# Performance work log

Measured on AMD Instinct MI355X. Metric: run time of the kernel, lower is better.

The kernel has to match this reference:

```python
import jax, jax.numpy as jnp
import numpy as np
import math

N_NODES = 20000
N_EDGES = 320000
NODE_IN = 128
HIDDEN = 64
HEADS = 4
TIME_DIM = 64
SCALE = 60.0 / 1.0  # sensitivity / epsilon


def _linear_params(key, din, dout):
    k1, k2 = jax.random.split(key)
    bound = 1.0 / math.sqrt(din)
    w = jax.random.uniform(k1, (din, dout), minval=-bound, maxval=bound, dtype=jnp.float32)
    b = jax.random.uniform(k2, (dout,), minval=-bound, maxval=bound, dtype=jnp.float32)
    return w, b


def setup_inputs() -> dict:
    key = jax.random.key(0)
    ks = jax.random.split(key, 16)
    edge_index = jax.random.randint(ks[0], (2, N_EDGES), 0, N_NODES, dtype=jnp.int64)
    raw_time = jax.random.uniform(ks[1], (N_EDGES, 1), dtype=jnp.float32) * 86400.0
    noise = jax.random.laplace(ks[2], (N_EDGES, 1), dtype=jnp.float32) * SCALE
    node_emb = jax.random.normal(ks[3], (N_NODES, NODE_IN), dtype=jnp.float32)
    HC = HEADS * HIDDEN
    wq1, bq1 = _linear_params(ks[4], NODE_IN, HC)
    wk1, bk1 = _linear_params(ks[5], NODE_IN, HC)
    wv1, bv1 = _linear_params(ks[6], NODE_IN, HC)
    wt1, bt1 = _linear_params(ks[7], TIME_DIM, HC)
    wq2, bq2 = _linear_params(ks[8], HC, HC)
    wk2, bk2 = _linear_params(ks[9], HC, HC)
    wv2, bv2 = _linear_params(ks[10], HC, HC)
    wt2, bt2 = _linear_params(ks[11], TIME_DIM, HC)
    wc, bc = _linear_params(ks[12], HC, 1)
    return dict(edge_index=edge_index, raw_time=raw_time, noise=noise, node_emb=node_emb,
                wq1=wq1, bq1=bq1, wk1=wk1, bk1=bk1, wv1=wv1, bv1=bv1, wt1=wt1, bt1=bt1,
                wq2=wq2, bq2=bq2, wk2=wk2, bk2=bk2, wv2=wv2, bv2=bv2, wt2=wt2, bt2=bt2,
                wc=wc, bc=bc)


def time_encode(t):
    # t: [E, 1] -> [E, TIME_DIM]; interleaved sin/cos as in TimeEncoder
    half = jnp.arange(0, TIME_DIM, 2, dtype=jnp.float32)
    div_term = jnp.exp(half * (-math.log(10000.0) / TIME_DIM))  # [TIME_DIM/2]
    arg = t * div_term  # [E, TIME_DIM/2]
    te = jnp.stack([jnp.sin(arg), jnp.cos(arg)], axis=-1)  # [E, T/2, 2]
    return te.reshape(t.shape[0], TIME_DIM)


def temporal_conv(x, src, dst, time_enc, wq, bq, wk, bk, wv, bv, wt, bt):
    # gather-QKV, edge softmax over dst segments, scatter-add aggregation
    N = x.shape[0]
    q = (x @ wq + bq).reshape(N, HEADS, HIDDEN)
    k = (x @ wk + bk).reshape(N, HEADS, HIDDEN)
    v = (x @ wv + bv).reshape(N, HEADS, HIDDEN)
    t_enc = (time_enc @ wt + bt).reshape(-1, HEADS, HIDDEN)  # [E,H,C]
    q_i = q[dst]                      # [E,H,C]
    k_j = k[src] + t_enc              # [E,H,C]
    alpha = (q_i * k_j).sum(-1) / math.sqrt(HIDDEN)  # [E,H]
    # segment softmax over index = dst (PyG softmax semantics)
    amax = jax.ops.segment_max(alpha, dst, num_segments=N)  # [N,H]
    ea = jnp.exp(alpha - amax[dst])
    denom = jax.ops.segment_sum(ea, dst, num_segments=N)
    alpha = ea / (denom[dst] + 1e-16)
    msg = v[src] * alpha[..., None]   # [E,H,C]
    out = jax.ops.segment_sum(msg, dst, num_segments=N)  # [N,H,C]
    return out.reshape(N, HEADS * HIDDEN)


def reference(edge_index, raw_time, noise, node_emb,
              wq1, bq1, wk1, bk1, wv1, bv1, wt1, bt1,
              wq2, bq2, wk2, bk2, wv2, bv2, wt2, bt2,
              wc, bc):
    src, dst = edge_index[0], edge_index[1]
    noisy_time = raw_time + noise                 # Laplace mechanism
    time_encoded = time_encode(noisy_time)        # [E, TIME_DIM]
    x = jax.nn.relu(temporal_conv(node_emb, src, dst, time_encoded,
                                  wq1, bq1, wk1, bk1, wv1, bv1, wt1, bt1))
    x = jax.nn.relu(temporal_conv(x, src, dst, time_encoded,
                                  wq2, bq2, wk2, bk2, wv2, bv2, wt2, bt2))
    edge_emb = x[src] + x[dst]                    # [E, H*C]
    out = edge_emb @ wc + bc                      # [E, 1]
    return out.squeeze(-1)
```

## Files before the change

### kernel.cpp

```cpp
#include <hip/hip_runtime.h>
#include <hip/hip_fp16.h>
#include <math.h>

#define NN   20000
#define NE   320000
#define NIN  128
#define HC   256
#define NB   1024

typedef unsigned short u16;
typedef __attribute__((ext_vector_type(8))) short bf16x8;
typedef __attribute__((ext_vector_type(8))) unsigned short u16x8;
typedef __attribute__((ext_vector_type(4))) float f32x4;

__device__ __forceinline__ float bf2f(u16 u) {
  union { unsigned int i; float f; } x;
  x.i = ((unsigned int)u) << 16;
  return x.f;
}
__device__ __forceinline__ u16 f2bf(float f) {
  union { float f; unsigned int i; } x;
  x.f = f;
  unsigned int r = x.i + 0x7fffu + ((x.i >> 16) & 1u);
  return (u16)(r >> 16);
}

__device__ __forceinline__ float ldf(const void* p, int i, bool fbf) {
  return fbf ? bf2f(((const u16*)p)[i]) : ((const float*)p)[i];
}
__device__ __forceinline__ int ldsrc(const void* p, int e, bool is64) {
  const int* p32 = (const int*)p;
  return is64 ? p32[2 * e] : p32[e];
}
__device__ __forceinline__ int lddst(const void* p, int e, bool is64) {
  const int* p32 = (const int*)p;
  return is64 ? p32[2 * (NE + e)] : p32[NE + e];
}
__device__ __forceinline__ void stout(void* p, int i, float v, bool fbf) {
  if (fbf) ((u16*)p)[i] = f2bf(v);
  else ((float*)p)[i] = v;
}

__device__ __forceinline__ void gload_lds16(const u16* g, u16* l) {
  __builtin_amdgcn_global_load_lds(
      (const __attribute__((address_space(1))) void*)g,
      (__attribute__((address_space(3))) void*)l, 16, 0, 0);
}

__global__ void devinit_kernel(const void* __restrict__ eidx,
                               const void* __restrict__ nemb,
                               int* __restrict__ flags, float* __restrict__ divt) {
  int lane = threadIdx.x;
  if (lane < 32) {
    const float c32 = (float)(-0.14391156831212787);
    float prod = (float)(2 * lane) * c32;
    divt[lane] = (float)exp((double)prod);
  }
  if (lane == 0) {
    const int* p32 = (const int*)eidx;
    int is64 = 1;
    for (int i = 1; i < 128; i += 2)
      if (p32[i] != 0) { is64 = 0; break; }
    const u16* q16 = (const u16*)nemb;
    int fbf = 1;
    for (int i = 0; i < 128; i += 2) {
      unsigned e = (q16[i] >> 7) & 0xFF;
      if (e < 90 || e > 140) { fbf = 0; break; }
    }
    flags[0] = is64;
    flags[1] = fbf;
  }
}

__global__ void sentinel_kernel(const int* __restrict__ flags, void* __restrict__ out) {
  int i = blockIdx.x * 256 + threadIdx.x;
  if (i < NE) stout(out, i, 3000.0f, flags[1] != 0);
}
__global__ void raw_sentinel_kernel(u16* __restrict__ out) {
  int i = blockIdx.x * 256 + threadIdx.x;
  if (i < NE) out[i] = f2bf(3000.0f);
}

__global__ void zero_kernel(int* __restrict__ p, int n) {
  int i = blockIdx.x * 256 + threadIdx.x;
  if (i < n) p[i] = 0;
}

__global__ void hist_kernel(const int* __restrict__ flags, const void* __restrict__ eidx,
                            int* __restrict__ cnt) {
  bool is64 = flags[0] != 0;
  int e = blockIdx.x * 256 + threadIdx.x;
  if (e < NE) {
    int d = lddst(eidx, e, is64);
    if ((unsigned)d < NN) atomicAdd(&cnt[d], 1);
  }
}

__global__ void scan1_kernel(const int* __restrict__ cnt, int* __restrict__ offs,
                             int* __restrict__ bsum, int n) {
  __shared__ int s[256];
  int b = blockIdx.x, t = threadIdx.x, i = b * 256 + t;
  int x = (i < n) ? cnt[i] : 0;
  s[t] = x;
  __syncthreads();
  for (int off = 1; off < 256; off <<= 1) {
    int y = (t >= off) ? s[t - off] : 0;
    __syncthreads();
    s[t] += y;
    __syncthreads();
  }
  if (i < n) offs[i] = s[t] - x;
  if (t == 255) bsum[b] = s[t];
}

__global__ void scan2_kernel(int* __restrict__ bsum, int* __restrict__ offs,
                             int nb, int n) {
  __shared__ int s[256];
  int t = threadIdx.x;
  int x = (t < nb) ? bsum[t] : 0;
  s[t] = x;
  __syncthreads();
  for (int off = 1; off < 256; off <<= 1) {
    int y = (t >= off) ? s[t - off] : 0;
    __syncthreads();
    s[t] += y;
    __syncthreads();
  }
  if (t < nb) bsum[t] = s[t] - x;
  if (t == 255) offs[n] = s[t];
}

__global__ void scan3_kernel(int* __restrict__ offs, const int* __restrict__ bsum,
                             int* __restrict__ cursor, int n) {
  int i = blockIdx.x * 256 + threadIdx.x;
  if (i < n) {
    int v = offs[i] + bsum[blockIdx.x];
    offs[i] = v;
    cursor[i] = v;
  }
}

__global__ void fill_kernel(const int* __restrict__ flags, const void* __restrict__ eidx,
                            const void* __restrict__ rawt, const void* __restrict__ noise,
                            int* __restrict__ cursor, int* __restrict__ ssrc,
                            float* __restrict__ stt) {
  bool is64 = flags[0] != 0, fbf = flags[1] != 0;
  int e = blockIdx.x * 256 + threadIdx.x;
  if (e < NE) {
    int d = lddst(eidx, e, is64);
    if ((unsigned)d < NN) {
      int pos = atomicAdd(&cursor[d], 1);
      if ((unsigned)pos < NE) {
        int src = ldsrc(eidx, e, is64);
        if ((unsigned)src >= NN) src = 0;
        ssrc[pos] = src;
        stt[pos] = ldf(rawt, e, fbf) + ldf(noise, e, fbf);
      }
    }
  }
}

__global__ __launch_bounds__(256) void te_kernel(
    const float* __restrict__ stt, const float* __restrict__ divt,
    u16* __restrict__ te_s) {
  int idx = blockIdx.x * 256 + threadIdx.x;
  int p = idx >> 5;
  if (p >= NE) return;
  int f = idx & 31;
  float tt = stt[p];
  float arg = tt * divt[f];
  double rev = (double)arg * 0.15915494309189535;
  double fr = rev - floor(rev);
  float red = (float)(fr * 6.283185307179586);
  float sv, cv;
  sincosf(red, &sv, &cv);
  __half hs = __float2half(sv), hc = __float2half(cv);
  unsigned int packed = (unsigned int)(*(u16*)&hs) | ((unsigned int)(*(u16*)&hc) << 16);
  ((unsigned int*)te_s)[(size_t)p * 32 + f] = packed;
}

__global__ void transw3_kernel(const int* __restrict__ flags, const void* __restrict__ W0,
                               const void* __restrict__ W1, const void* __restrict__ W2,
                               u16* __restrict__ WtBig, int K) {
  bool fbf = flags[1] != 0;
  __shared__ u16 tile[64][65];
  int z = blockIdx.z;
  const void* W = (z == 0) ? W0 : (z == 1) ? W1 : W2;
  u16* dst = WtBig + (size_t)z * 256 * K;
  int kb = blockIdx.x * 64, cb = blockIdx.y * 64;
  int tx = threadIdx.x & 63, ty = threadIdx.x >> 6;
  for (int i = ty; i < 64; i += 4)
    tile[tx][i] = f2bf(ldf(W, (kb + i) * HC + cb + tx, fbf));
  __syncthreads();
  for (int i = ty; i < 64; i += 4)
    dst[(size_t)(cb + i) * K + kb + tx] = tile[i][tx];
}

__global__ void wcombbias_kernel(const int* __restrict__ flags, const void* __restrict__ wt,
                                 const u16* __restrict__ Wqt, u16* __restrict__ Wout,
                                 const void* __restrict__ bq, const void* __restrict__ bk,
                                 const void* __restrict__ bv, float* __restrict__ biasBig,
                                 int K) {
  bool fbf = flags[1] != 0;
  int b = blockIdx.x, t = threadIdx.x;
  if (b < 256) {
    __shared__ float wrow[64];
    int j = b, h = j >> 6;
    if (t < 64) wrow[t] = ldf(wt, (j & 63) * HC + h * 64 + t, fbf);
    __syncthreads();
    if (t < K) {
      float s = 0.f;
#pragma unroll 8
      for (int mm = 0; mm < 64; ++mm)
        s += wrow[mm] * bf2f(Wqt[(size_t)(h * 64 + mm) * K + t]);
      Wout[(size_t)j * K + t] = f2bf(s);
    }
  } else if (b < 259) {
    int bb = b - 256;
    const void* p = (bb == 0) ? bq : (bb == 1) ? bk : bv;
    biasBig[bb * 256 + t] = ldf(p, t, fbf);
  } else {
    int j = t, h = j >> 6;
    float s = 0.f;
    for (int mm = 0; mm < 64; ++mm)
      s += ldf(bq, h * 64 + mm, fbf) * ldf(wt, (j & 63) * HC + h * 64 + mm, fbf);
    biasBig[768 + j] = s;
  }
}

template <bool AWS>
__global__ __launch_bounds__(256) void gemm_mfma(
    const int* __restrict__ flags, const void* __restrict__ Ap,
    const u16* __restrict__ Wt, const float* __restrict__ bias,
    u16* __restrict__ C, int M, int K) {
  bool fbf = flags[1] != 0;
  __shared__ u16 As[128 * 32];
  __shared__ u16 Bs[128 * 32];
  int tid = threadIdx.x;
  int rb = blockIdx.x * 128, cb = blockIdx.y * 128;
  int wave = tid >> 6, lane = tid & 63;
  int l15 = lane & 15, quad = lane >> 4;
  int mbase = (wave >> 1) * 64, nbase = (wave & 1) * 64;

  f32x4 acc[4][4];
#pragma unroll
  for (int mt = 0; mt < 4; ++mt)
#pragma unroll
    for (int nt = 0; nt < 4; ++nt)
#pragma unroll
      for (int r = 0; r < 4; ++r) acc[mt][nt][r] = 0.f;

  int srow0 = tid >> 2, schunk0 = tid & 3;
  int srow1 = (tid + 256) >> 2, schunk1 = (tid + 256) & 3;
  int gchunk0 = schunk0 ^ (srow0 & 3);
  int gchunk1 = schunk1 ^ (srow1 & 3);
  int arow0 = rb + srow0; if (arow0 >= M) arow0 = M - 1;
  int arow1 = rb + srow1; if (arow1 >= M) arow1 = M - 1;
  u16* asl0 = &As[srow0 * 32 + schunk0 * 8];
  u16* asl1 = &As[srow1 * 32 + schunk1 * 8];
  u16* bsl0 = &Bs[srow0 * 32 + schunk0 * 8];
  u16* bsl1 = &Bs[srow1 * 32 + schunk1 * 8];
  const u16* bsrc0 = Wt + (size_t)(cb + srow0) * K + gchunk0 * 8;
  const u16* bsrc1 = Wt + (size_t)(cb + srow1) * K + gchunk1 * 8;
  const bool adirect = AWS || fbf;
  const u16* asrc0 = adirect ? ((const u16*)Ap + (size_t)arow0 * K + gchunk0 * 8) : (const u16*)0;
  const u16* asrc1 = adirect ? ((const u16*)Ap + (size_t)arow1 * K + gchunk1 * 8) : (const u16*)0;

  for (int kk = 0; kk < K; kk += 32) {
    if (adirect) {
      gload_lds16(asrc0 + kk, asl0);
      gload_lds16(asrc1 + kk, asl1);
    } else {
      const float* A0 = (const float*)Ap + (size_t)arow0 * K + kk + gchunk0 * 8;
      const float* A1 = (const float*)Ap + (size_t)arow1 * K + kk + gchunk1 * 8;
      bf16x8 t0, t1;
#pragma unroll
      for (int i = 0; i < 8; ++i) { t0[i] = (short)f2bf(A0[i]); t1[i] = (short)f2bf(A1[i]); }
      *(bf16x8*)asl0 = t0;
      *(bf16x8*)asl1 = t1;
    }
    gload_lds16(bsrc0 + kk, bsl0);
    gload_lds16(bsrc1 + kk, bsl1);
    __syncthreads();

    bf16x8 bfrag[4];
#pragma unroll
    for (int nt = 0; nt < 4; ++nt) {
      int col = nbase + nt * 16 + l15;
      bfrag[nt] = *(const bf16x8*)&Bs[col * 32 + ((quad ^ (col & 3)) * 8)];
    }
#pragma unroll
    for (int mt = 0; mt < 4; ++mt) {
      int row = mbase + mt * 16 + l15;
      bf16x8 afrag = *(const bf16x8*)&As[row * 32 + ((quad ^ (row & 3)) * 8)];
#pragma unroll
      for (int nt = 0; nt < 4; ++nt)
        acc[mt][nt] = __builtin_amdgcn_mfma_f32_16x16x32_bf16(afrag, bfrag[nt], acc[mt][nt], 0, 0, 0);
    }
    __syncthreads();
  }

#pragma unroll
  for (int nt = 0; nt < 4; ++nt) {
    int gcol = cb + nbase + nt * 16 + l15;
    float bv = bias[gcol];
    int scol;
    if (gcol < 256) scol = gcol;
    else if (gcol < 512) { int cc = gcol - 256; scol = 256 + ((cc >> 2) << 3) + (cc & 3); }
    else if (gcol < 768) { int cc = gcol - 512; scol = 256 + ((cc >> 2) << 3) + 4 + (cc & 3); }
    else scol = gcol;
#pragma unroll
    for (int mt = 0; mt < 4; ++mt) {
#pragma unroll
      for (int r = 0; r < 4; ++r) {
        int grow = rb + mbase + mt * 16 + quad * 4 + r;
        if (grow < M) C[(size_t)grow * NB + scol] = f2bf(acc[mt][nt][r] + bv);
      }
    }
  }
}

template <int DOY>
__global__ __launch_bounds__(256) void aggfused_kernel(
    const int* __restrict__ flags, const int* __restrict__ ssrc,
    const int* __restrict__ offsets, const u16* __restrict__ te_s,
    const u16* __restrict__ qkvp, const void* __restrict__ bt,
    u16* __restrict__ xout, const void* __restrict__ wc,
    float* __restrict__ ynode) {
  bool fbf = flags[1] != 0;
  int w = threadIdx.x >> 6;
  int n = blockIdx.x * 4 + w;
  if (n >= NN) return;
  int lane = threadIdx.x & 63;
  int c = lane * 4;
  int s0 = offsets[n], s1 = offsets[n + 1];
  if (s0 < 0) s0 = 0;
  if (s1 > NE) s1 = NE;

  ushort4 q4 = *(const ushort4*)(qkvp + (size_t)n * NB + c);
  ushort4 p4 = *(const ushort4*)(qkvp + (size_t)n * NB + 768 + c);
  float qx = bf2f(q4.x), qy = bf2f(q4.y), qz = bf2f(q4.z), qw = bf2f(q4.w);
  float px = bf2f(p4.x), py = bf2f(p4.y), pz = bf2f(p4.z), pw = bf2f(p4.w);
  float pb = qx * ldf(bt, c + 0, fbf);
  pb += qy * ldf(bt, c + 1, fbf);
  pb += qz * ldf(bt, c + 2, fbf);
  pb += qw * ldf(bt, c + 3, fbf);
  pb += __shfl_xor(pb, 1);
  pb += __shfl_xor(pb, 2);
  pb += __shfl_xor(pb, 4);
  pb += __shfl_xor(pb, 8);
  float qb = pb;
  int jb = c & 63;
  int kvoff = 256 + lane * 8;

  float m = -INFINITY, denom = 0.f;
  float acc0 = 0.f, acc1 = 0.f, acc2 = 0.f, acc3 = 0.f;

#define ALPHA_OF(kv, t4, out_a, okflag)                                        \
  {                                                                            \
    float s = qx * bf2f((kv)[0]) + __half2float(*(__half*)&(t4).x) * px;       \
    s += qy * bf2f((kv)[1]) + __half2float(*(__half*)&(t4).y) * py;            \
    s += qz * bf2f((kv)[2]) + __half2float(*(__half*)&(t4).z) * pz;            \
    s += qw * bf2f((kv)[3]) + __half2float(*(__half*)&(t4).w) * pw;            \
    s += __shfl_xor(s, 1);                                                     \
    s += __shfl_xor(s, 2);                                                     \
    s += __shfl_xor(s, 4);                                                     \
    s += __shfl_xor(s, 8);                                                     \
    out_a = (okflag) ? (s + qb) * 0.125f : 0.f;                                \
  }

#define STATE_UPDATE(a, kv, okflag)                                            \
  {                                                                            \
    float ea;                                                                  \
    if ((a) > m) {                                                             \
      float sc = __expf(m - (a));                                              \
      denom *= sc;                                                             \
      acc0 *= sc; acc1 *= sc; acc2 *= sc; acc3 *= sc;                          \
      m = (a);                                                                 \
      ea = 1.0f;                                                               \
    } else {                                                                   \
      ea = __expf((a) - m);                                                    \
    }                                                                          \
    denom += ea;                                                               \
    if (okflag) {                                                              \
      acc0 += ea * bf2f((kv)[4]);                                              \
      acc1 += ea * bf2f((kv)[5]);                                              \
      acc2 += ea * bf2f((kv)[6]);                                              \
      acc3 += ea * bf2f((kv)[7]);                                              \
    }                                                                          \
  }

  int p = s0;
  for (; p + 3 < s1; p += 4) {
    int srcA = ssrc[p], srcB = ssrc[p + 1], srcC = ssrc[p + 2], srcD = ssrc[p + 3];
    bool okA = (unsigned)srcA < NN, okB = (unsigned)srcB < NN;
    bool okC = (unsigned)srcC < NN, okD = (unsigned)srcD < NN;
    if (!okA) srcA = 0;
    if (!okB) srcB = 0;
    if (!okC) srcC = 0;
    if (!okD) srcD = 0;
    u16x8 kvA = *(const u16x8*)(qkvp + (size_t)srcA * NB + kvoff);
    u16x8 kvB = *(const u16x8*)(qkvp + (size_t)srcB * NB + kvoff);
    u16x8 kvC = *(const u16x8*)(qkvp + (size_t)srcC * NB + kvoff);
    u16x8 kvD = *(const u16x8*)(qkvp + (size_t)srcD * NB + kvoff);
    ushort4 tA = *(const ushort4*)(te_s + (size_t)p * 64 + jb);
    ushort4 tB = *(const ushort4*)(te_s + (size_t)(p + 1) * 64 + jb);
    ushort4 tC = *(const ushort4*)(te_s + (size_t)(p + 2) * 64 + jb);
    ushort4 tD = *(const ushort4*)(te_s + (size_t)(p + 3) * 64 + jb);

    float aA, aB, aC, aD;
    ALPHA_OF(kvA, tA, aA, okA)
    ALPHA_OF(kvB, tB, aB, okB)
    ALPHA_OF(kvC, tC, aC, okC)
    ALPHA_OF(kvD, tD, aD, okD)
    STATE_UPDATE(aA, kvA, okA)
    STATE_UPDATE(aB, kvB, okB)
    STATE_UPDATE(aC, kvC, okC)
    STATE_UPDATE(aD, kvD, okD)
  }
  for (; p < s1; ++p) {
    int src = ssrc[p];
    bool ok = (unsigned)src < NN;
    if (!ok) src = 0;
    u16x8 kv = *(const u16x8*)(qkvp + (size_t)src * NB + kvoff);
    ushort4 t4 = *(const ushort4*)(te_s + (size_t)p * 64 + jb);
    float a;
    ALPHA_OF(kv, t4, a, ok)
    STATE_UPDATE(a, kv, ok)
  }
#undef ALPHA_OF
#undef STATE_UPDATE

  float inv = 1.f / (denom + 1e-16f);
  ushort4 r;
  r.x = f2bf(fmaxf(acc0 * inv, 0.f));
  r.y = f2bf(fmaxf(acc1 * inv, 0.f));
  r.z = f2bf(fmaxf(acc2 * inv, 0.f));
  r.w = f2bf(fmaxf(acc3 * inv, 0.f));
  *(ushort4*)(xout + (size_t)n * HC + c) = r;
  if (DOY) {
    float yv = bf2f(r.x) * ldf(wc, c + 0, fbf);
    yv += bf2f(r.y) * ldf(wc, c + 1, fbf);
    yv += bf2f(r.z) * ldf(wc, c + 2, fbf);
    yv += bf2f(r.w) * ldf(wc, c + 3, fbf);
    for (int off = 32; off; off >>= 1) yv += __shfl_xor(yv, off);
    if (lane == 0) ynode[n] = yv;
  }
}

__global__ __launch_bounds__(256) void final2_kernel(
    const int* __restrict__ flags, const void* __restrict__ eidx,
    const float* __restrict__ y, const void* __restrict__ bc,
    void* __restrict__ out) {
  bool is64 = flags[0] != 0, fbf = flags[1] != 0;
  int e = blockIdx.x * 256 + threadIdx.x;
  if (e >= NE) return;
  int src = ldsrc(eidx, e, is64);
  int dst = lddst(eidx, e, is64);
  if ((unsigned)src >= NN) src = 0;
  if ((unsigned)dst >= NN) dst = 0;
  stout(out, e, y[src] + y[dst] + ldf(bc, 0, fbf), fbf);
}

extern "C" void kernel_launch(void* const* d_in, const int* in_sizes, int n_in,
                              void* d_out, int out_size, void* d_ws, size_t ws_size,
                              hipStream_t stream) {
  const void* eidx  = d_in[0];
  const void* rawt  = d_in[1];
  const void* noise = d_in[2];
  const void* nemb  = d_in[3];
  const void *wq1 = d_in[4],  *bq1 = d_in[5];
  const void *wk1 = d_in[6],  *bk1 = d_in[7];
  const void *wv1 = d_in[8],  *bv1 = d_in[9];
  const void *wt1 = d_in[10], *bt1 = d_in[11];
  const void *wq2 = d_in[12], *bq2 = d_in[13];
  const void *wk2 = d_in[14], *bk2 = d_in[15];
  const void *wv2 = d_in[16], *bv2 = d_in[17];
  const void *wt2 = d_in[18], *bt2 = d_in[19];
  const void *wcp = d_in[20], *bcp = d_in[21];

  char* ws = (char*)d_ws;
  size_t off = 0;
  auto alloc = [&](size_t bytes) -> void* {
    void* p = ws + off;
    off += (bytes + 255) & ~(size_t)255;
    return p;
  };
  int*   flags  = (int*)alloc(256);
  float* divt   = (float*)alloc(256);
  u16*   WtBig  = (u16*)alloc((size_t)NB * HC * 2);
  float* biasBig= (float*)alloc((size_t)NB * 4);
  u16*   qkvp   = (u16*)alloc((size_t)NN * NB * 2);
  u16*   x1     = (u16*)alloc((size_t)NN * HC * 2);
  u16*   x2     = (u16*)alloc((size_t)NN * HC * 2);
  float* ynode  = (float*)alloc((size_t)NN * 4);
  int* offsets  = (int*)alloc((size_t)(NN + 1) * 4);
  int* cursor   = (int*)alloc((size_t)NN * 4);
  int* bsum     = (int*)alloc(256 * 4);
  int* ssrc     = (int*)alloc((size_t)NE * 4);
  float* stt    = (float*)alloc((size_t)NE * 4);
  u16* te_s     = (u16*)alloc((size_t)NE * 64 * 2);
  size_t need = off;

  int gN = (NN + 255) / 256, gE = (NE + 255) / 256;
  int nb = (NN + 255) / 256;

  if (ws_size < 1024) {
    raw_sentinel_kernel<<<gE, 256, 0, stream>>>((u16*)d_out);
    return;
  }
  devinit_kernel<<<1, 64, 0, stream>>>(eidx, nemb, flags, divt);
  if (need > ws_size) {
    sentinel_kernel<<<gE, 256, 0, stream>>>(flags, d_out);
    return;
  }

  zero_kernel<<<gN, 256, 0, stream>>>(cursor, NN);
  hist_kernel<<<gE, 256, 0, stream>>>(flags, eidx, cursor);
  scan1_kernel<<<nb, 256, 0, stream>>>(cursor, offsets, bsum, NN);
  scan2_kernel<<<1, 256, 0, stream>>>(bsum, offsets, nb, NN);
  scan3_kernel<<<nb, 256, 0, stream>>>(offsets, bsum, cursor, NN);
  fill_kernel<<<gE, 256, 0, stream>>>(flags, eidx, rawt, noise, cursor, ssrc, stt);

  int gTe = (NE * 32 + 255) / 256;
  te_kernel<<<gTe, 256, 0, stream>>>(stt, divt, te_s);

  dim3 ggemm((NN + 127) / 128, NB / 128);
  dim3 gt1(NIN / 64, 4, 3), gt2(HC / 64, 4, 3);
  int gNode = (NN + 3) / 4;

  transw3_kernel<<<gt1, 256, 0, stream>>>(flags, wq1, wk1, wv1, WtBig, NIN);
  wcombbias_kernel<<<260, 256, 0, stream>>>(flags, wt1, WtBig, WtBig + (size_t)768 * NIN,
                                            bq1, bk1, bv1, biasBig, NIN);
  gemm_mfma<false><<<ggemm, 256, 0, stream>>>(flags, nemb, WtBig, biasBig, qkvp, NN, NIN);
  aggfused_kernel<0><<<gNode, 256, 0, stream>>>(flags, ssrc, offsets, te_s, qkvp, bt1,
                                                x1, wcp, ynode);

  transw3_kernel<<<gt2, 256, 0, stream>>>(flags, wq2, wk2, wv2, WtBig, HC);
  wcombbias_kernel<<<260, 256, 0, stream>>>(flags, wt2, WtBig, WtBig + (size_t)768 * HC,
                                            bq2, bk2, bv2, biasBig, HC);
  gemm_mfma<true><<<ggemm, 256, 0, stream>>>(flags, x1, WtBig, biasBig, qkvp, NN, HC);
  aggfused_kernel<1><<<gNode, 256, 0, stream>>>(flags, ssrc, offsets, te_s, qkvp, bt2,
                                                x2, wcp, ynode);

  final2_kernel<<<gE, 256, 0, stream>>>(flags, eidx, ynode, bcp, d_out);
}
```

Baseline: 391.4 us.

## Make edge aggregation a persistent work-queue kernel with max-free exp2 softmax

The per-node aggregation kernel becomes a persistent grid of 2048 blocks. Each wave claims its next node through an atomic counter and prefetches that node's offsets and q/p rows while it processes the current one. The online-max softmax rescaling is removed, and scores are pre-scaled by log2e/8 so a raw hardware exp2 can be used. Reductions now use DPP row sums, and the QK dot product uses bf16 dot2. The time-encoding kernel switches to hardware sin/cos on a revolution-normalised argument. Dropping the max subtraction risks overflow when scores are large, and the hardware sin/cos change slightly alters numerics.

```diff
diff --git a/kernel.cpp b/kernel.cpp
--- a/kernel.cpp
+++ b/kernel.cpp
@@ -8,6 +8,10 @@
 #define HC   256
 #define NB   1024
 
+#define AGG_BLOCKS 2048
+#define AGG_WAVES  (AGG_BLOCKS * 4)
+#define LOG2E_8    0.18033688f
+
 typedef unsigned short u16;
 typedef __attribute__((ext_vector_type(8))) short bf16x8;
 typedef __attribute__((ext_vector_type(8))) unsigned short u16x8;
@@ -24,6 +28,12 @@
   unsigned int r = x.i + 0x7fffu + ((x.i >> 16) & 1u);
   return (u16)(r >> 16);
 }
+__device__ __forceinline__ float bflo(int v) {
+  union { int i; float f; } x; x.i = v << 16; return x.f;
+}
+__device__ __forceinline__ float bfhi(int v) {
+  union { int i; float f; } x; x.i = v & 0xffff0000; return x.f;
+}
 
 __device__ __forceinline__ float ldf(const void* p, int i, bool fbf) {
   return fbf ? bf2f(((const u16*)p)[i]) : ((const float*)p)[i];
@@ -45,6 +55,59 @@
   __builtin_amdgcn_global_load_lds(
       (const __attribute__((address_space(1))) void*)g,
       (__attribute__((address_space(3))) void*)l, 16, 0, 0);
+}
+
+__device__ __forceinline__ float dpp_row_allsum(float s) {
+  union fi { float f; int i; };
+  fi a, b;
+  a.f = s;
+  b.i = __builtin_amdgcn_update_dpp(0, a.i, 0x121, 0xf, 0xf, true); a.f += b.f;
+  b.i = __builtin_amdgcn_update_dpp(0, a.i, 0x122, 0xf, 0xf, true); a.f += b.f;
+  b.i = __builtin_amdgcn_update_dpp(0, a.i, 0x124, 0xf, 0xf, true); a.f += b.f;
+  b.i = __builtin_amdgcn_update_dpp(0, a.i, 0x128, 0xf, 0xf, true); a.f += b.f;
+  return a.f;
+}
+
+__device__ __forceinline__ float fexp2(float x) {
+#if __has_builtin(__builtin_amdgcn_exp2f)
+  return __builtin_amdgcn_exp2f(x);
+#else
+  return exp2f(x);
+#endif
+}
+
+#if __has_builtin(__builtin_amdgcn_fdot2_f32_bf16)
+#define HAS_BF16_DOT2 1
+typedef __attribute__((ext_vector_type(2))) __bf16 bfv2_t;
+__device__ __forceinline__ float qkdot2(int a, int b, float c) {
+  return __builtin_amdgcn_fdot2_f32_bf16(__builtin_bit_cast(bfv2_t, a),
+                                         __builtin_bit_cast(bfv2_t, b), c, false);
+}
+#else
+#define HAS_BF16_DOT2 0
+#endif
+
+__device__ __forceinline__ void edge_do(int4 kv, int2 t, int2 q2,
+    float qsx, float qsy, float qsz, float qsw,
+    float px, float py, float pz, float pw, float qb,
+    float& denom, float& a0, float& a1, float& a2, float& a3) {
+  float2 f01 = __half22float2(__builtin_bit_cast(__half2, t.x));
+  float2 f23 = __half22float2(__builtin_bit_cast(__half2, t.y));
+  float stp = f01.x * px + f01.y * py + f23.x * pz + f23.y * pw;
+#if HAS_BF16_DOT2
+  float sqk = qkdot2(kv.y, q2.y, qkdot2(kv.x, q2.x, 0.f));
+  float partial = sqk * LOG2E_8 + stp;
+#else
+  float partial = stp + qsx * bflo(kv.x) + qsy * bfhi(kv.x) +
+                  qsz * bflo(kv.y) + qsw * bfhi(kv.y);
+#endif
+  float a = dpp_row_allsum(partial) + qb;
+  float ea = fexp2(a);
+  denom += ea;
+  a0 = fmaf(ea, bflo(kv.z), a0);
+  a1 = fmaf(ea, bfhi(kv.z), a1);
+  a2 = fmaf(ea, bflo(kv.w), a2);
+  a3 = fmaf(ea, bfhi(kv.w), a3);
 }
 
 __global__ void devinit_kernel(const void* __restrict__ eidx,
@@ -69,6 +132,8 @@
     }
     flags[0] = is64;
     flags[1] = fbf;
+    flags[2] = AGG_WAVES;
+    flags[3] = AGG_WAVES;
   }
 }
 
@@ -171,9 +236,9 @@
   float arg = tt * divt[f];
   double rev = (double)arg * 0.15915494309189535;
   double fr = rev - floor(rev);
-  float red = (float)(fr * 6.283185307179586);
-  float sv, cv;
-  sincosf(red, &sv, &cv);
+  float frf = (float)fr;
+  float sv = __builtin_amdgcn_sinf(frf);
+  float cv = __builtin_amdgcn_cosf(frf);
   __half hs = __float2half(sv), hc = __float2half(cv);
   unsigned int packed = (unsigned int)(*(u16*)&hs) | ((unsigned int)(*(u16*)&hc) << 16);
   ((unsigned int*)te_s)[(size_t)p * 32 + f] = packed;
@@ -321,130 +386,107 @@
 }
 
 template <int DOY>
-__global__ __launch_bounds__(256) void aggfused_kernel(
+__global__ __launch_bounds__(256, 4) void aggfused_kernel(
     const int* __restrict__ flags, const int* __restrict__ ssrc,
     const int* __restrict__ offsets, const u16* __restrict__ te_s,
     const u16* __restrict__ qkvp, const void* __restrict__ bt,
     u16* __restrict__ xout, const void* __restrict__ wc,
-    float* __restrict__ ynode) {
+    float* __restrict__ ynode, int* __restrict__ qctr) {
   bool fbf = flags[1] != 0;
-  int w = threadIdx.x >> 6;
-  int n = blockIdx.x * 4 + w;
-  if (n >= NN) return;
   int lane = threadIdx.x & 63;
   int c = lane * 4;
-  int s0 = offsets[n], s1 = offsets[n + 1];
-  if (s0 < 0) s0 = 0;
-  if (s1 > NE) s1 = NE;
-
-  ushort4 q4 = *(const ushort4*)(qkvp + (size_t)n * NB + c);
-  ushort4 p4 = *(const ushort4*)(qkvp + (size_t)n * NB + 768 + c);
-  float qx = bf2f(q4.x), qy = bf2f(q4.y), qz = bf2f(q4.z), qw = bf2f(q4.w);
-  float px = bf2f(p4.x), py = bf2f(p4.y), pz = bf2f(p4.z), pw = bf2f(p4.w);
-  float pb = qx * ldf(bt, c + 0, fbf);
-  pb += qy * ldf(bt, c + 1, fbf);
-  pb += qz * ldf(bt, c + 2, fbf);
-  pb += qw * ldf(bt, c + 3, fbf);
-  pb += __shfl_xor(pb, 1);
-  pb += __shfl_xor(pb, 2);
-  pb += __shfl_xor(pb, 4);
-  pb += __shfl_xor(pb, 8);
-  float qb = pb;
   int jb = c & 63;
   int kvoff = 256 + lane * 8;
 
-  float m = -INFINITY, denom = 0.f;
-  float acc0 = 0.f, acc1 = 0.f, acc2 = 0.f, acc3 = 0.f;
-
-#define ALPHA_OF(kv, t4, out_a, okflag)                                        \
-  {                                                                            \
-    float s = qx * bf2f((kv)[0]) + __half2float(*(__half*)&(t4).x) * px;       \
-    s += qy * bf2f((kv)[1]) + __half2float(*(__half*)&(t4).y) * py;            \
-    s += qz * bf2f((kv)[2]) + __half2float(*(__half*)&(t4).z) * pz;            \
-    s += qw * bf2f((kv)[3]) + __half2float(*(__half*)&(t4).w) * pw;            \
-    s += __shfl_xor(s, 1);                                                     \
-    s += __shfl_xor(s, 2);                                                     \
-    s += __shfl_xor(s, 4);                                                     \
-    s += __shfl_xor(s, 8);                                                     \
-    out_a = (okflag) ? (s + qb) * 0.125f : 0.f;                                \
-  }
-
-#define STATE_UPDATE(a, kv, okflag)                                            \
-  {                                                                            \
-    float ea;                                                                  \
-    if ((a) > m) {                                                             \
-      float sc = __expf(m - (a));                                              \
-      denom *= sc;                                                             \
-      acc0 *= sc; acc1 *= sc; acc2 *= sc; acc3 *= sc;                          \
-      m = (a);                                                                 \
-      ea = 1.0f;                                                               \
-    } else {                                                                   \
-      ea = __expf((a) - m);                                                    \
-    }                                                                          \
-    denom += ea;                                                               \
-    if (okflag) {                                                              \
-      acc0 += ea * bf2f((kv)[4]);                                              \
-      acc1 += ea * bf2f((kv)[5]);                                              \
-      acc2 += ea * bf2f((kv)[6]);                                              \
-      acc3 += ea * bf2f((kv)[7]);                                              \
-    }                                                                          \
-  }
-
-  int p = s0;
-  for (; p + 3 < s1; p += 4) {
-    int srcA = ssrc[p], srcB = ssrc[p + 1], srcC = ssrc[p + 2], srcD = ssrc[p + 3];
-    bool okA = (unsigned)srcA < NN, okB = (unsigned)srcB < NN;
-    bool okC = (unsigned)srcC < NN, okD = (unsigned)srcD < NN;
-    if (!okA) srcA = 0;
-    if (!okB) srcB = 0;
-    if (!okC) srcC = 0;
-    if (!okD) srcD = 0;
-    u16x8 kvA = *(const u16x8*)(qkvp + (size_t)srcA * NB + kvoff);
-    u16x8 kvB = *(const u16x8*)(qkvp + (size_t)srcB * NB + kvoff);
-    u16x8 kvC = *(const u16x8*)(qkvp + (size_t)srcC * NB + kvoff);
-    u16x8 kvD = *(const u16x8*)(qkvp + (size_t)srcD * NB + kvoff);
-    ushort4 tA = *(const ushort4*)(te_s + (size_t)p * 64 + jb);
-    ushort4 tB = *(const ushort4*)(te_s + (size_t)(p + 1) * 64 + jb);
-    ushort4 tC = *(const ushort4*)(te_s + (size_t)(p + 2) * 64 + jb);
-    ushort4 tD = *(const ushort4*)(te_s + (size_t)(p + 3) * 64 + jb);
-
-    float aA, aB, aC, aD;
-    ALPHA_OF(kvA, tA, aA, okA)
-    ALPHA_OF(kvB, tB, aB, okB)
-    ALPHA_OF(kvC, tC, aC, okC)
-    ALPHA_OF(kvD, tD, aD, okD)
-    STATE_UPDATE(aA, kvA, okA)
-    STATE_UPDATE(aB, kvB, okB)
-    STATE_UPDATE(aC, kvC, okC)
-    STATE_UPDATE(aD, kvD, okD)
-  }
-  for (; p < s1; ++p) {
-    int src = ssrc[p];
-    bool ok = (unsigned)src < NN;
-    if (!ok) src = 0;
-    u16x8 kv = *(const u16x8*)(qkvp + (size_t)src * NB + kvoff);
-    ushort4 t4 = *(const ushort4*)(te_s + (size_t)p * 64 + jb);
-    float a;
-    ALPHA_OF(kv, t4, a, ok)
-    STATE_UPDATE(a, kv, ok)
-  }
-#undef ALPHA_OF
-#undef STATE_UPDATE
-
-  float inv = 1.f / (denom + 1e-16f);
-  ushort4 r;
-  r.x = f2bf(fmaxf(acc0 * inv, 0.f));
-  r.y = f2bf(fmaxf(acc1 * inv, 0.f));
-  r.z = f2bf(fmaxf(acc2 * inv, 0.f));
-  r.w = f2bf(fmaxf(acc3 * inv, 0.f));
-  *(ushort4*)(xout + (size_t)n * HC + c) = r;
+  float btv0 = ldf(bt, c + 0, fbf), btv1 = ldf(bt, c + 1, fbf);
+  float btv2 = ldf(bt, c + 2, fbf), btv3 = ldf(bt, c + 3, fbf);
+  float wcv0 = 0.f, wcv1 = 0.f, wcv2 = 0.f, wcv3 = 0.f;
   if (DOY) {
-    float yv = bf2f(r.x) * ldf(wc, c + 0, fbf);
-    yv += bf2f(r.y) * ldf(wc, c + 1, fbf);
-    yv += bf2f(r.z) * ldf(wc, c + 2, fbf);
-    yv += bf2f(r.w) * ldf(wc, c + 3, fbf);
-    for (int off = 32; off; off >>= 1) yv += __shfl_xor(yv, off);
-    if (lane == 0) ynode[n] = yv;
+    wcv0 = ldf(wc, c + 0, fbf); wcv1 = ldf(wc, c + 1, fbf);
+    wcv2 = ldf(wc, c + 2, fbf); wcv3 = ldf(wc, c + 3, fbf);
+  }
+
+  int n = blockIdx.x * 4 + (threadIdx.x >> 6);
+  int s0 = offsets[n], s1 = offsets[n + 1];
+  int2 q2 = *(const int2*)(qkvp + (size_t)n * NB + c);
+  int2 p2 = *(const int2*)(qkvp + (size_t)n * NB + 768 + c);
+  int pg = NN;
+  if (lane == 0) pg = atomicAdd(qctr, 1);
+
+  while (n < NN) {
+    int gnew = NN;
+    if (lane == 0) gnew = atomicAdd(qctr, 1);
+    int n1 = __builtin_amdgcn_readfirstlane(pg);
+    int n1c = (n1 < NN) ? n1 : 0;
+    int s0n = offsets[n1c], s1n = offsets[n1c + 1];
+    int2 q2n = *(const int2*)(qkvp + (size_t)n1c * NB + c);
+    int2 p2n = *(const int2*)(qkvp + (size_t)n1c * NB + 768 + c);
+
+    float qx = bflo(q2.x), qy = bfhi(q2.x), qz = bflo(q2.y), qw = bfhi(q2.y);
+    float px = bflo(p2.x) * LOG2E_8, py = bfhi(p2.x) * LOG2E_8;
+    float pz = bflo(p2.y) * LOG2E_8, pw = bfhi(p2.y) * LOG2E_8;
+    float pb = qx * btv0 + qy * btv1 + qz * btv2 + qw * btv3;
+    float qb = dpp_row_allsum(pb) * LOG2E_8;
+    float qsx = qx * LOG2E_8, qsy = qy * LOG2E_8;
+    float qsz = qz * LOG2E_8, qsw = qw * LOG2E_8;
+
+    float denom = 0.f, acc0 = 0.f, acc1 = 0.f, acc2 = 0.f, acc3 = 0.f;
+    const int* sp = ssrc + s0;
+    const u16* tep = te_s + (size_t)s0 * 64 + jb;
+    int ecnt = s1 - s0;
+    int e = 0;
+    if (ecnt >= 4) {
+      int sA = sp[0], sB = sp[1], sC = sp[2], sD = sp[3];
+      while (e + 4 <= ecnt) {
+        int4 kvA = *(const int4*)(qkvp + ((unsigned)(sA << 10) + (unsigned)kvoff));
+        int4 kvB = *(const int4*)(qkvp + ((unsigned)(sB << 10) + (unsigned)kvoff));
+        int4 kvC = *(const int4*)(qkvp + ((unsigned)(sC << 10) + (unsigned)kvoff));
+        int4 kvD = *(const int4*)(qkvp + ((unsigned)(sD << 10) + (unsigned)kvoff));
+        int2 tA = *(const int2*)(tep + (size_t)e * 64);
+        int2 tB = *(const int2*)(tep + (size_t)(e + 1) * 64);
+        int2 tC = *(const int2*)(tep + (size_t)(e + 2) * 64);
+        int2 tD = *(const int2*)(tep + (size_t)(e + 3) * 64);
+        int en = e + 4;
+        if (en + 4 <= ecnt) {
+          sA = sp[en]; sB = sp[en + 1]; sC = sp[en + 2]; sD = sp[en + 3];
+        }
+        edge_do(kvA, tA, q2, qsx, qsy, qsz, qsw, px, py, pz, pw, qb,
+                denom, acc0, acc1, acc2, acc3);
+        edge_do(kvB, tB, q2, qsx, qsy, qsz, qsw, px, py, pz, pw, qb,
+                denom, acc0, acc1, acc2, acc3);
+        edge_do(kvC, tC, q2, qsx, qsy, qsz, qsw, px, py, pz, pw, qb,
+                denom, acc0, acc1, acc2, acc3);
+        edge_do(kvD, tD, q2, qsx, qsy, qsz, qsw, px, py, pz, pw, qb,
+                denom, acc0, acc1, acc2, acc3);
+        e = en;
+      }
+    }
+    for (; e < ecnt; ++e) {
+      int s = sp[e];
+      int4 kv = *(const int4*)(qkvp + ((unsigned)(s << 10) + (unsigned)kvoff));
+      int2 t = *(const int2*)(tep + (size_t)e * 64);
+      edge_do(kv, t, q2, qsx, qsy, qsz, qsw, px, py, pz, pw, qb,
+              denom, acc0, acc1, acc2, acc3);
+    }
+
+    float inv = 1.f / (denom + 1e-16f);
+    ushort4 r;
+    r.x = f2bf(fmaxf(acc0 * inv, 0.f));
+    r.y = f2bf(fmaxf(acc1 * inv, 0.f));
+    r.z = f2bf(fmaxf(acc2 * inv, 0.f));
+    r.w = f2bf(fmaxf(acc3 * inv, 0.f));
+    *(ushort4*)(xout + (size_t)n * HC + c) = r;
+    if (DOY) {
+      float yv = bf2f(r.x) * wcv0 + bf2f(r.y) * wcv1 +
+                 bf2f(r.z) * wcv2 + bf2f(r.w) * wcv3;
+      yv = dpp_row_allsum(yv);
+      yv += __shfl_xor(yv, 16);
+      yv += __shfl_xor(yv, 32);
+      if (lane == 0) ynode[n] = yv;
+    }
+
+    n = n1; pg = gnew;
+    s0 = s0n; s1 = s1n; q2 = q2n; p2 = p2n;
   }
 }
 
@@ -527,21 +569,20 @@
 
   dim3 ggemm((NN + 127) / 128, NB / 128);
   dim3 gt1(NIN / 64, 4, 3), gt2(HC / 64, 4, 3);
-  int gNode = (NN + 3) / 4;
 
   transw3_kernel<<<gt1, 256, 0, stream>>>(flags, wq1, wk1, wv1, WtBig, NIN);
   wcombbias_kernel<<<260, 256, 0, stream>>>(flags, wt1, WtBig, WtBig + (size_t)768 * NIN,
                                             bq1, bk1, bv1, biasBig, NIN);
   gemm_mfma<false><<<ggemm, 256, 0, stream>>>(flags, nemb, WtBig, biasBig, qkvp, NN, NIN);
-  aggfused_kernel<0><<<gNode, 256, 0, stream>>>(flags, ssrc, offsets, te_s, qkvp, bt1,
-                                                x1, wcp, ynode);
+  aggfused_kernel<0><<<AGG_BLOCKS, 256, 0, stream>>>(flags, ssrc, offsets, te_s, qkvp, bt1,
+                                                     x1, wcp, ynode, flags + 2);
 
   transw3_kernel<<<gt2, 256, 0, stream>>>(flags, wq2, wk2, wv2, WtBig, HC);
   wcombbias_kernel<<<260, 256, 0, stream>>>(flags, wt2, WtBig, WtBig + (size_t)768 * HC,
                                             bq2, bk2, bv2, biasBig, HC);
   gemm_mfma<true><<<ggemm, 256, 0, stream>>>(flags, x1, WtBig, biasBig, qkvp, NN, HC);
-  aggfused_kernel<1><<<gNode, 256, 0, stream>>>(flags, ssrc, offsets, te_s, qkvp, bt2,
-                                                x2, wcp, ynode);
+  aggfused_kernel<1><<<AGG_BLOCKS, 256, 0, stream>>>(flags, ssrc, offsets, te_s, qkvp, bt2,
+                                                     x2, wcp, ynode, flags + 3);
 
   final2_kernel<<<gE, 256, 0, stream>>>(flags, eidx, ynode, bcp, d_out);
 }
```

Result: slower. 956.4 us (+144.4%).
